# Kernel tuning notes

Hardware: AMD Instinct MI355X
Metric: run time of the kernel (lower is better)

Reference implementation:

```python
import jax, jax.numpy as jnp
import numpy as np

N_NODES = 524288
BLOCK = 128
NUM_BLOCKS = N_NODES // BLOCK  # 4096
MAX_KV = 64
GRAPH_WEIGHT = 0.3


def setup_inputs() -> dict:
    key = jax.random.key(0)
    k1, k2, k3, k4, k5, k6 = jax.random.split(key, 6)
    logits = jax.random.normal(k1, (N_NODES, 1), dtype=jnp.float32)
    targets = jax.random.randint(k2, (N_NODES, 1), 0, 2).astype(jnp.float32)
    sup_mask = jax.random.bernoulli(k3, 0.2, (N_NODES,))
    ignore_mask = jax.random.bernoulli(k4, 0.1, (N_NODES,))
    kv_indices = jax.random.randint(k5, (NUM_BLOCKS, MAX_KV), 0, NUM_BLOCKS, dtype=jnp.int32)
    kv_num_blocks = jax.random.randint(k6, (NUM_BLOCKS,), 1, MAX_KV + 1, dtype=jnp.int32)
    return {
        "logits": logits,
        "targets": targets,
        "sup_mask": sup_mask,
        "ignore_mask": ignore_mask,
        "kv_indices": kv_indices,
        "kv_num_blocks": kv_num_blocks,
        "block_size": BLOCK,
    }


def reference(logits, targets, sup_mask, ignore_mask, kv_indices, kv_num_blocks, block_size):
    x = logits[:, 0]
    t = targets[:, 0]

    # --- supervised BCE-with-logits, masked mean over sup_mask ---
    # BCEWithLogits(x, t) = softplus(x) - t * x
    bce = jax.nn.softplus(x) - t * x
    sup_f = sup_mask.astype(x.dtype)
    sup_cnt = sup_f.sum()
    loss_sup = jnp.where(sup_cnt > 0, (bce * sup_f).sum() / jnp.maximum(sup_cnt, 1.0), 0.0)

    # --- blockwise graph smoothness loss ---
    p = jax.nn.sigmoid(x)
    nb = x.shape[0] // block_size
    p_blk = p.reshape(nb, block_size)                         # [nb, B]
    uncertain = (~ignore_mask) & (~sup_mask)
    unc_blk = uncertain.reshape(nb, block_size)               # [nb, B]
    keep_blk = (~ignore_mask).reshape(nb, block_size)         # [nb, B]

    max_kv = kv_indices.shape[1]
    kv_valid = jnp.arange(max_kv, dtype=kv_num_blocks.dtype)[None, :] < kv_num_blocks[:, None]  # [nb, K]

    neigh_p = p_blk[kv_indices]                               # [nb, K, B] block-sparse gather
    neigh_keep = keep_blk[kv_indices] & kv_valid[:, :, None]  # [nb, K, B]
    nk_f = neigh_keep.astype(p.dtype)
    n_cnt = nk_f.sum(axis=(1, 2))                             # [nb]
    n_mean = (neigh_p * nk_f).sum(axis=(1, 2)) / jnp.maximum(n_cnt, 1.0)  # [nb]

    unc_f = unc_blk.astype(p.dtype)
    q_cnt = unc_f.sum(axis=1)                                 # [nb]
    sq = ((p_blk - n_mean[:, None]) ** 2) * unc_f             # [nb, B]
    blk_loss = sq.sum(axis=1) / jnp.maximum(q_cnt, 1.0)       # [nb]

    valid = ((q_cnt > 0) & (n_cnt > 0)).astype(p.dtype)
    count = valid.sum()
    loss_graph = (blk_loss * valid).sum() / jnp.maximum(count, 1.0)

    return loss_sup + GRAPH_WEIGHT * loss_graph
```

## Files before the change

### kernel.cpp

```cpp
#include <hip/hip_runtime.h>
#include <stdint.h>

#define N_NODES 524288
#define BLOCK 128
#define NUM_BLOCKS 4096
#define MAX_KV 64
#define GRAPH_WEIGHT 0.3f

#define WS_SUMP 0
#define WS_CNTK 4096
#define WS_QCNT 8192
#define WS_BCEP 12288
#define WS_SUPP 16384
#define WS_GNUM 20480
#define WS_GCNT 24576

__device__ __forceinline__ bool read_mask(const void* p, int i, int byteflag) {
    if (byteflag) return ((const uint8_t*)p)[i] != 0;
    return ((const int*)p)[i] != 0;
}

__device__ __forceinline__ int detect_byteflag(const void* sup, int t, int* sh_flag) {
    if (t == 0) *sh_flag = 0;
    __syncthreads();
    const unsigned int* w = (const unsigned int*)sup;
    unsigned int a = w[t] | w[t + 128];
    if (a > 1u) *sh_flag = 1;
    __syncthreads();
    return *sh_flag;
}

__global__ void __launch_bounds__(BLOCK)
k1_per_block(const float* __restrict__ logits, const float* __restrict__ targets,
             const void* __restrict__ sup, const void* __restrict__ ign,
             float* __restrict__ ws) {
    const int b = blockIdx.x, t = threadIdx.x;
    const int i = b * BLOCK + t;
    __shared__ int sh_flag;
    const int bf = detect_byteflag(sup, t, &sh_flag);
    float x  = logits[i];
    float tg = targets[i];
    bool s = read_mask(sup, i, bf);
    bool g = read_mask(ign, i, bf);
    float bce = fmaxf(x, 0.f) + log1pf(expf(-fabsf(x))) - tg * x;
    float p = 1.f / (1.f + expf(-x));
    float v0 = g ? 0.f : p;
    float v1 = g ? 0.f : 1.f;
    float v2 = (!g && !s) ? 1.f : 0.f;
    float v3 = s ? bce : 0.f;
    float v4 = s ? 1.f : 0.f;
    for (int off = 32; off > 0; off >>= 1) {
        v0 += __shfl_down(v0, off);
        v1 += __shfl_down(v1, off);
        v2 += __shfl_down(v2, off);
        v3 += __shfl_down(v3, off);
        v4 += __shfl_down(v4, off);
    }
    __shared__ float sh[2][5];
    if ((t & 63) == 0) {
        int w = t >> 6;
        sh[w][0] = v0; sh[w][1] = v1; sh[w][2] = v2; sh[w][3] = v3; sh[w][4] = v4;
    }
    __syncthreads();
    if (t == 0) {
        ws[WS_SUMP + b] = sh[0][0] + sh[1][0];
        ws[WS_CNTK + b] = sh[0][1] + sh[1][1];
        ws[WS_QCNT + b] = sh[0][2] + sh[1][2];
        ws[WS_BCEP + b] = sh[0][3] + sh[1][3];
        ws[WS_SUPP + b] = sh[0][4] + sh[1][4];
    }
}

__global__ void __launch_bounds__(BLOCK)
k2_graph(const float* __restrict__ logits,
         const void* __restrict__ sup, const void* __restrict__ ign,
         const int* __restrict__ kvi, const int* __restrict__ kvn,
         float* __restrict__ ws) {
    const int b = blockIdx.x, t = threadIdx.x;
    __shared__ int sh_flag;
    const int bf = detect_byteflag(sup, t, &sh_flag);
    __shared__ float sh_nmean, sh_ncnt;
    if (t < 64) {
        float ns = 0.f, nc = 0.f;
        int num = kvn[b];
        if (t < num) {
            int j = kvi[b * MAX_KV + t];
            ns = ws[WS_SUMP + j];
            nc = ws[WS_CNTK + j];
        }
        for (int off = 32; off > 0; off >>= 1) {
            ns += __shfl_down(ns, off);
            nc += __shfl_down(nc, off);
        }
        if (t == 0) {
            sh_ncnt  = nc;
            sh_nmean = ns / fmaxf(nc, 1.f);
        }
    }
    __syncthreads();
    const float nmean = sh_nmean;
    const float ncnt  = sh_ncnt;
    const int i = b * BLOCK + t;
    float x = logits[i];
    bool s = read_mask(sup, i, bf);
    bool g = read_mask(ign, i, bf);
    float p = 1.f / (1.f + expf(-x));
    float d = p - nmean;
    float v = (!g && !s) ? d * d : 0.f;
    for (int off = 32; off > 0; off >>= 1)
        v += __shfl_down(v, off);
    __shared__ float shv[2];
    if ((t & 63) == 0) shv[t >> 6] = v;
    __syncthreads();
    if (t == 0) {
        float vs = shv[0] + shv[1];
        float qc = ws[WS_QCNT + b];
        bool valid = (qc > 0.f) && (ncnt > 0.f);
        ws[WS_GNUM + b] = valid ? vs / fmaxf(qc, 1.f) : 0.f;
        ws[WS_GCNT + b] = valid ? 1.f : 0.f;
    }
}

__global__ void __launch_bounds__(256)
k3_final(const float* __restrict__ ws, float* __restrict__ out) {
    const int t = threadIdx.x;
    float bce = 0.f, scnt = 0.f, gnum = 0.f, gcnt = 0.f;
    for (int b = t; b < NUM_BLOCKS; b += 256) {
        bce  += ws[WS_BCEP + b];
        scnt += ws[WS_SUPP + b];
        gnum += ws[WS_GNUM + b];
        gcnt += ws[WS_GCNT + b];
    }
    for (int off = 32; off > 0; off >>= 1) {
        bce  += __shfl_down(bce, off);
        scnt += __shfl_down(scnt, off);
        gnum += __shfl_down(gnum, off);
        gcnt += __shfl_down(gcnt, off);
    }
    __shared__ float sh[4][4];
    if ((t & 63) == 0) {
        int w = t >> 6;
        sh[w][0] = bce; sh[w][1] = scnt; sh[w][2] = gnum; sh[w][3] = gcnt;
    }
    __syncthreads();
    if (t == 0) {
        float bs = sh[0][0] + sh[1][0] + sh[2][0] + sh[3][0];
        float sc = sh[0][1] + sh[1][1] + sh[2][1] + sh[3][1];
        float gn = sh[0][2] + sh[1][2] + sh[2][2] + sh[3][2];
        float gc = sh[0][3] + sh[1][3] + sh[2][3] + sh[3][3];
        float loss_sup = (sc > 0.f) ? bs / fmaxf(sc, 1.f) : 0.f;
        float loss_graph = gn / fmaxf(gc, 1.f);
        out[0] = loss_sup + GRAPH_WEIGHT * loss_graph;
    }
}

extern "C" void kernel_launch(void* const* d_in, const int* in_sizes, int n_in,
                              void* d_out, int out_size, void* d_ws, size_t ws_size,
                              hipStream_t stream) {
    const float* logits  = (const float*)d_in[0];
    const float* targets = (const float*)d_in[1];
    const void*  sup     = d_in[2];
    const void*  ign     = d_in[3];
    const int*   kvi     = (const int*)d_in[4];
    const int*   kvn     = (const int*)d_in[5];
    float* out = (float*)d_out;
    float* ws  = (float*)d_ws;

    k1_per_block<<<NUM_BLOCKS, BLOCK, 0, stream>>>(logits, targets, sup, ign, ws);
    k2_graph<<<NUM_BLOCKS, BLOCK, 0, stream>>>(logits, sup, ign, kvi, kvn, ws);
    k3_final<<<1, 256, 0, stream>>>(ws, out);
}
```

Baseline: 82.49 us.

## Fuse three kernels into one persistent kernel with a grid barrier

Replaces the three-kernel pipeline with a single kernel of 512 workgroups. Each workgroup handles 8 blocks, keeps the probabilities in registers, publishes per-block neighbour sums, and waits at a software grid-wide barrier (atomic counter plus spin) before doing the neighbour gather. A last-block-done atomic then performs the final reduction. This removes two kernel launches and the recomputation or reload of logits and masks in the second pass. In exchange it adds a memset, relies on all 512 workgroups being co-resident to avoid deadlock, and adds many __syncthreads in the per-iteration reductions.

```diff
diff --git a/kernel.cpp b/kernel.cpp
--- a/kernel.cpp
+++ b/kernel.cpp
@@ -7,150 +7,188 @@
 #define MAX_KV 64
 #define GRAPH_WEIGHT 0.3f
 
-#define WS_SUMP 0
-#define WS_CNTK 4096
-#define WS_QCNT 8192
-#define WS_BCEP 12288
-#define WS_SUPP 16384
-#define WS_GNUM 20480
-#define WS_GCNT 24576
-
-__device__ __forceinline__ bool read_mask(const void* p, int i, int byteflag) {
-    if (byteflag) return ((const uint8_t*)p)[i] != 0;
+#define GRID 512
+#define THREADS 256
+#define NB_PER_WG (NUM_BLOCKS / GRID)
+#define ITERS (NB_PER_WG * BLOCK / THREADS)
+
+#define WS_SUMP 16
+#define WS_CNTK (WS_SUMP + NUM_BLOCKS)
+#define WS_BCE  (WS_CNTK + NUM_BLOCKS)
+#define WS_SUP  (WS_BCE + GRID)
+#define WS_GNUM (WS_SUP + GRID)
+#define WS_GCNT (WS_GNUM + GRID)
+
+__device__ __forceinline__ bool read_mask(const void* p, int i, int bf) {
+    if (bf) return ((const uint8_t*)p)[i] != 0;
     return ((const int*)p)[i] != 0;
 }
 
-__device__ __forceinline__ int detect_byteflag(const void* sup, int t, int* sh_flag) {
-    if (t == 0) *sh_flag = 0;
-    __syncthreads();
-    const unsigned int* w = (const unsigned int*)sup;
-    unsigned int a = w[t] | w[t + 128];
-    if (a > 1u) *sh_flag = 1;
-    __syncthreads();
-    return *sh_flag;
-}
-
-__global__ void __launch_bounds__(BLOCK)
-k1_per_block(const float* __restrict__ logits, const float* __restrict__ targets,
-             const void* __restrict__ sup, const void* __restrict__ ign,
-             float* __restrict__ ws) {
-    const int b = blockIdx.x, t = threadIdx.x;
-    const int i = b * BLOCK + t;
+__global__ void __launch_bounds__(THREADS, 2)
+k_fused(const float* __restrict__ logits, const float* __restrict__ targets,
+        const void* __restrict__ sup, const void* __restrict__ ign,
+        const int* __restrict__ kvi, const int* __restrict__ kvn,
+        float* __restrict__ ws, float* __restrict__ out) {
+    const int wg = blockIdx.x, t = threadIdx.x;
+    const int lane = t & 63, wave = t >> 6;
+    unsigned* cnt = (unsigned*)ws;
+
     __shared__ int sh_flag;
-    const int bf = detect_byteflag(sup, t, &sh_flag);
-    float x  = logits[i];
-    float tg = targets[i];
-    bool s = read_mask(sup, i, bf);
-    bool g = read_mask(ign, i, bf);
-    float bce = fmaxf(x, 0.f) + log1pf(expf(-fabsf(x))) - tg * x;
-    float p = 1.f / (1.f + expf(-x));
-    float v0 = g ? 0.f : p;
-    float v1 = g ? 0.f : 1.f;
-    float v2 = (!g && !s) ? 1.f : 0.f;
-    float v3 = s ? bce : 0.f;
-    float v4 = s ? 1.f : 0.f;
+    if (t == 0) sh_flag = 0;
+    __syncthreads();
+    {
+        const unsigned* w = (const unsigned*)sup;
+        if (w[t] > 1u) sh_flag = 1;
+    }
+    __syncthreads();
+    const int bf = sh_flag;
+
+    __shared__ float sh_red[4][4];
+    __shared__ float sh_qcnt[NB_PER_WG];
+    __shared__ float sh_nmean[NB_PER_WG];
+    __shared__ float sh_ncnt[NB_PER_WG];
+    __shared__ int sh_last;
+
+    float pj[ITERS];
+    float uj[ITERS];
+    float bce_acc = 0.f, sup_acc = 0.f;
+
+    const int base = wg * (NB_PER_WG * BLOCK);
+
+    #pragma unroll
+    for (int j = 0; j < ITERS; ++j) {
+        const int i = base + j * THREADS + t;
+        const float x  = logits[i];
+        const float tg = targets[i];
+        const bool s = read_mask(sup, i, bf);
+        const bool g = read_mask(ign, i, bf);
+        const float bce = fmaxf(x, 0.f) + log1pf(expf(-fabsf(x))) - tg * x;
+        const float p = 1.f / (1.f + expf(-x));
+        pj[j] = p;
+        const float u = (!g && !s) ? 1.f : 0.f;
+        uj[j] = u;
+        if (s) { bce_acc += bce; sup_acc += 1.f; }
+
+        float v0 = g ? 0.f : p;
+        float v1 = g ? 0.f : 1.f;
+        float v2 = u;
+        for (int off = 32; off > 0; off >>= 1) {
+            v0 += __shfl_down(v0, off);
+            v1 += __shfl_down(v1, off);
+            v2 += __shfl_down(v2, off);
+        }
+        if (lane == 0) { sh_red[wave][0] = v0; sh_red[wave][1] = v1; sh_red[wave][2] = v2; }
+        __syncthreads();
+        if (t < 2) {
+            const int nbl = j * 2 + t;
+            const int nb  = wg * NB_PER_WG + nbl;
+            ws[WS_SUMP + nb] = sh_red[2*t][0] + sh_red[2*t+1][0];
+            ws[WS_CNTK + nb] = sh_red[2*t][1] + sh_red[2*t+1][1];
+            sh_qcnt[nbl]     = sh_red[2*t][2] + sh_red[2*t+1][2];
+        }
+        __syncthreads();
+    }
+
     for (int off = 32; off > 0; off >>= 1) {
-        v0 += __shfl_down(v0, off);
-        v1 += __shfl_down(v1, off);
-        v2 += __shfl_down(v2, off);
-        v3 += __shfl_down(v3, off);
-        v4 += __shfl_down(v4, off);
-    }
-    __shared__ float sh[2][5];
-    if ((t & 63) == 0) {
-        int w = t >> 6;
-        sh[w][0] = v0; sh[w][1] = v1; sh[w][2] = v2; sh[w][3] = v3; sh[w][4] = v4;
-    }
+        bce_acc += __shfl_down(bce_acc, off);
+        sup_acc += __shfl_down(sup_acc, off);
+    }
+    if (lane == 0) { sh_red[wave][0] = bce_acc; sh_red[wave][1] = sup_acc; }
     __syncthreads();
     if (t == 0) {
-        ws[WS_SUMP + b] = sh[0][0] + sh[1][0];
-        ws[WS_CNTK + b] = sh[0][1] + sh[1][1];
-        ws[WS_QCNT + b] = sh[0][2] + sh[1][2];
-        ws[WS_BCEP + b] = sh[0][3] + sh[1][3];
-        ws[WS_SUPP + b] = sh[0][4] + sh[1][4];
-    }
-}
-
-__global__ void __launch_bounds__(BLOCK)
-k2_graph(const float* __restrict__ logits,
-         const void* __restrict__ sup, const void* __restrict__ ign,
-         const int* __restrict__ kvi, const int* __restrict__ kvn,
-         float* __restrict__ ws) {
-    const int b = blockIdx.x, t = threadIdx.x;
-    __shared__ int sh_flag;
-    const int bf = detect_byteflag(sup, t, &sh_flag);
-    __shared__ float sh_nmean, sh_ncnt;
-    if (t < 64) {
+        ws[WS_BCE + wg] = sh_red[0][0] + sh_red[1][0] + sh_red[2][0] + sh_red[3][0];
+        ws[WS_SUP + wg] = sh_red[0][1] + sh_red[1][1] + sh_red[2][1] + sh_red[3][1];
+    }
+
+    __syncthreads();
+    if (t == 0) {
+        __threadfence();
+        atomicAdd(&cnt[0], 1u);
+        while (__hip_atomic_load(&cnt[0], __ATOMIC_RELAXED,
+                                 __HIP_MEMORY_SCOPE_AGENT) < (unsigned)GRID)
+            __builtin_amdgcn_s_sleep(1);
+    }
+    __syncthreads();
+    __threadfence();
+
+    #pragma unroll
+    for (int r = 0; r < 2; ++r) {
+        const int nbl = r * 4 + wave;
+        const int nb  = wg * NB_PER_WG + nbl;
         float ns = 0.f, nc = 0.f;
-        int num = kvn[b];
-        if (t < num) {
-            int j = kvi[b * MAX_KV + t];
-            ns = ws[WS_SUMP + j];
-            nc = ws[WS_CNTK + j];
+        const int num = kvn[nb];
+        if (lane < num) {
+            const int jj = kvi[nb * MAX_KV + lane];
+            ns = ws[WS_SUMP + jj];
+            nc = ws[WS_CNTK + jj];
         }
         for (int off = 32; off > 0; off >>= 1) {
             ns += __shfl_down(ns, off);
             nc += __shfl_down(nc, off);
         }
+        if (lane == 0) { sh_ncnt[nbl] = nc; sh_nmean[nbl] = ns / fmaxf(nc, 1.f); }
+    }
+    __syncthreads();
+
+    float gnum_acc = 0.f, gcnt_acc = 0.f;
+    #pragma unroll
+    for (int j = 0; j < ITERS; ++j) {
+        const int nbl = j * 2 + (t >> 7);
+        const float d = pj[j] - sh_nmean[nbl];
+        float v = uj[j] * d * d;
+        for (int off = 32; off > 0; off >>= 1) v += __shfl_down(v, off);
+        if (lane == 0) sh_red[wave][0] = v;
+        __syncthreads();
+        if (t < 2) {
+            const int nbl2 = j * 2 + t;
+            const float vs = sh_red[2*t][0] + sh_red[2*t+1][0];
+            const float qc = sh_qcnt[nbl2];
+            const bool valid = (qc > 0.f) && (sh_ncnt[nbl2] > 0.f);
+            gnum_acc += valid ? vs / fmaxf(qc, 1.f) : 0.f;
+            gcnt_acc += valid ? 1.f : 0.f;
+        }
+        __syncthreads();
+    }
+    gnum_acc += __shfl_down(gnum_acc, 1);
+    gcnt_acc += __shfl_down(gcnt_acc, 1);
+    if (t == 0) { ws[WS_GNUM + wg] = gnum_acc; ws[WS_GCNT + wg] = gcnt_acc; }
+
+    __syncthreads();
+    if (t == 0) {
+        __threadfence();
+        const unsigned old = atomicAdd(&cnt[1], 1u);
+        sh_last = (old == (unsigned)GRID - 1) ? 1 : 0;
+    }
+    __syncthreads();
+    if (sh_last) {
+        __threadfence();
+        float b = 0.f, sc = 0.f, gn = 0.f, gc = 0.f;
+        for (int w2 = t; w2 < GRID; w2 += THREADS) {
+            b  += ws[WS_BCE + w2];
+            sc += ws[WS_SUP + w2];
+            gn += ws[WS_GNUM + w2];
+            gc += ws[WS_GCNT + w2];
+        }
+        for (int off = 32; off > 0; off >>= 1) {
+            b  += __shfl_down(b, off);
+            sc += __shfl_down(sc, off);
+            gn += __shfl_down(gn, off);
+            gc += __shfl_down(gc, off);
+        }
+        if (lane == 0) {
+            sh_red[wave][0] = b; sh_red[wave][1] = sc;
+            sh_red[wave][2] = gn; sh_red[wave][3] = gc;
+        }
+        __syncthreads();
         if (t == 0) {
-            sh_ncnt  = nc;
-            sh_nmean = ns / fmaxf(nc, 1.f);
-        }
-    }
-    __syncthreads();
-    const float nmean = sh_nmean;
-    const float ncnt  = sh_ncnt;
-    const int i = b * BLOCK + t;
-    float x = logits[i];
-    bool s = read_mask(sup, i, bf);
-    bool g = read_mask(ign, i, bf);
-    float p = 1.f / (1.f + expf(-x));
-    float d = p - nmean;
-    float v = (!g && !s) ? d * d : 0.f;
-    for (int off = 32; off > 0; off >>= 1)
-        v += __shfl_down(v, off);
-    __shared__ float shv[2];
-    if ((t & 63) == 0) shv[t >> 6] = v;
-    __syncthreads();
-    if (t == 0) {
-        float vs = shv[0] + shv[1];
-        float qc = ws[WS_QCNT + b];
-        bool valid = (qc > 0.f) && (ncnt > 0.f);
-        ws[WS_GNUM + b] = valid ? vs / fmaxf(qc, 1.f) : 0.f;
-        ws[WS_GCNT + b] = valid ? 1.f : 0.f;
-    }
-}
-
-__global__ void __launch_bounds__(256)
-k3_final(const float* __restrict__ ws, float* __restrict__ out) {
-    const int t = threadIdx.x;
-    float bce = 0.f, scnt = 0.f, gnum = 0.f, gcnt = 0.f;
-    for (int b = t; b < NUM_BLOCKS; b += 256) {
-        bce  += ws[WS_BCEP + b];
-        scnt += ws[WS_SUPP + b];
-        gnum += ws[WS_GNUM + b];
-        gcnt += ws[WS_GCNT + b];
-    }
-    for (int off = 32; off > 0; off >>= 1) {
-        bce  += __shfl_down(bce, off);
-        scnt += __shfl_down(scnt, off);
-        gnum += __shfl_down(gnum, off);
-        gcnt += __shfl_down(gcnt, off);
-    }
-    __shared__ float sh[4][4];
-    if ((t & 63) == 0) {
-        int w = t >> 6;
-        sh[w][0] = bce; sh[w][1] = scnt; sh[w][2] = gnum; sh[w][3] = gcnt;
-    }
-    __syncthreads();
-    if (t == 0) {
-        float bs = sh[0][0] + sh[1][0] + sh[2][0] + sh[3][0];
-        float sc = sh[0][1] + sh[1][1] + sh[2][1] + sh[3][1];
-        float gn = sh[0][2] + sh[1][2] + sh[2][2] + sh[3][2];
-        float gc = sh[0][3] + sh[1][3] + sh[2][3] + sh[3][3];
-        float loss_sup = (sc > 0.f) ? bs / fmaxf(sc, 1.f) : 0.f;
-        float loss_graph = gn / fmaxf(gc, 1.f);
-        out[0] = loss_sup + GRAPH_WEIGHT * loss_graph;
+            const float B  = sh_red[0][0]+sh_red[1][0]+sh_red[2][0]+sh_red[3][0];
+            const float S  = sh_red[0][1]+sh_red[1][1]+sh_red[2][1]+sh_red[3][1];
+            const float GN = sh_red[0][2]+sh_red[1][2]+sh_red[2][2]+sh_red[3][2];
+            const float GC = sh_red[0][3]+sh_red[1][3]+sh_red[2][3]+sh_red[3][3];
+            const float loss_sup   = (S > 0.f) ? B / fmaxf(S, 1.f) : 0.f;
+            const float loss_graph = GN / fmaxf(GC, 1.f);
+            out[0] = loss_sup + GRAPH_WEIGHT * loss_graph;
+        }
     }
 }
 
@@ -166,7 +204,6 @@
     float* out = (float*)d_out;
     float* ws  = (float*)d_ws;
 
-    k1_per_block<<<NUM_BLOCKS, BLOCK, 0, stream>>>(logits, targets, sup, ign, ws);
-    k2_graph<<<NUM_BLOCKS, BLOCK, 0, stream>>>(logits, sup, ign, kvi, kvn, ws);
-    k3_final<<<1, 256, 0, stream>>>(ws, out);
+    hipMemsetAsync(d_ws, 0, 16, stream);
+    k_fused<<<GRID, THREADS, 0, stream>>>(logits, targets, sup, ign, kvi, kvn, ws, out);
 }
```

After: 141.6 us. +71.7%, slower.
